# Kernel optimization log

Measured on AMD Instinct MI355X. Metric: run time of the kernel, lower is better.

The kernel has to match this reference:

```python
import jax, jax.numpy as jnp
import numpy as np

B, H, W, BLK = 32, 512, 512, 8
QF_MIN, QF_MAX, QF_BIAS = 2.0, 50.0, 0.0

_RGB2YCC = jnp.array([[0.299, 0.587, 0.114],
                      [-0.168736, -0.331264, 0.5],
                      [0.5, -0.418688, -0.081312]], jnp.float32)
_YCC_OFF = jnp.array([0.0, 128.0, 128.0], jnp.float32)

Y_QTB = jnp.array([16,11,10,16,24,40,51,61,12,12,14,19,26,58,60,55,14,13,16,24,40,57,69,56,
                   14,17,22,29,51,87,80,62,18,22,37,56,68,109,103,77,24,36,55,64,81,104,113,92,
                   49,64,78,87,103,121,120,101,72,92,95,98,112,100,103,99], jnp.float32).reshape(8, 8)
C_QTB = jnp.array([17,18,24,47,99,99,99,99,18,21,26,66,99,99,99,99,24,26,56,99,99,99,99,99,
                   47,66,99,99,99,99,99,99,99,99,99,99,99,99,99,99,99,99,99,99,99,99,99,99,
                   99,99,99,99,99,99,99,99,99,99,99,99,99,99,99,99], jnp.float32).reshape(8, 8)

# orthonormal 8x8 DCT-II matrix
_k = np.arange(8.0)[:, None]; _n = np.arange(8.0)[None, :]
_C = 0.5 * np.cos((2 * _n + 1) * _k * np.pi / 16.0)
_C[0] *= 1.0 / np.sqrt(2.0)
DCT_M = jnp.asarray(_C, jnp.float32)

# standard JPEG zig-zag raster order over the 64 coefficients of an 8x8 block
ZIGZAG = jnp.array([0,1,8,16,9,2,3,10,17,24,32,25,18,11,4,5,12,19,26,33,40,48,41,34,27,20,13,6,
                    7,14,21,28,35,42,49,56,57,50,43,36,29,22,15,23,30,37,44,51,58,59,52,45,38,31,
                    39,46,53,60,61,54,47,55,62,63], jnp.int32)


def hard_round(x):
    # straight-through round: forward = round(x), backward = identity
    return x + jax.lax.stop_gradient(jnp.round(x) - x)


def split_blocks(x):
    # [B,H,W] -> [B,H/8,W/8,8,8]
    b, h, w = x.shape
    return x.reshape(b, h // BLK, BLK, w // BLK, BLK).transpose(0, 1, 3, 2, 4)


def dct2d(x):
    # 2D DCT over the trailing 8x8 dims: C @ X @ C^T
    return jnp.einsum('ij,bnmjk,lk->bnmil', DCT_M, x, DCT_M)


def _norm01(e):
    mn = e.min(axis=(1, 2), keepdims=True)
    mx = e.max(axis=(1, 2), keepdims=True)
    return (e - mn) / (mx - mn + 1e-6)


def _ac_energy(d):
    # per-block log AC energy, shape [B,h8,w8]
    return jnp.log1p(jnp.sum(d * d, axis=(-2, -1)) - d[..., 0, 0] ** 2 + 1e-6)


def _forward(rgb):
    ycbcr = hard_round(jnp.einsum('bhwc,kc->bhwk', rgb, _RGB2YCC) + _YCC_OFF) - 128.0
    y_d = dct2d(split_blocks(ycbcr[..., 0]))
    cb_d = dct2d(split_blocks(ycbcr[..., 1]))
    cr_d = dct2d(split_blocks(ycbcr[..., 2]))

    # QFMapGenerator (default): per-block AC-energy rank in [0,1], upsampled to pixels
    rank = jnp.stack([_norm01(_ac_energy(y_d)),
                      _norm01(0.5 * (_ac_energy(cb_d) + _ac_energy(cr_d)))], axis=-1)  # [B,h8,w8,2]
    rank_px = jnp.repeat(jnp.repeat(rank, BLK, axis=1), BLK, axis=2)  # [B,H,W,2]

    # RankToQF
    enc_qf = jnp.clip(hard_round(QF_MIN + rank_px * (QF_MAX - QF_MIN) + QF_BIAS), QF_MIN, QF_MAX)
    y_qf_min = enc_qf[..., 0].min(axis=(1, 2), keepdims=True)
    y_qf_max = enc_qf[..., 0].max(axis=(1, 2), keepdims=True)
    c_qf_min = enc_qf[..., 1].min(axis=(1, 2), keepdims=True)
    c_qf_max = enc_qf[..., 1].max(axis=(1, 2), keepdims=True)

    # QFToScale: standard JPEG QF -> scale factor
    enc_scale = hard_round(jnp.where(enc_qf < 50.0, 5000.0 / enc_qf, 200.0 - 2.0 * enc_qf)) / 100.0

    sy = split_blocks(enc_scale[..., 0])  # [B,h8,w8,8,8]
    sc = split_blocks(enc_scale[..., 1])
    yq = hard_round(y_d / (sy * Y_QTB))
    cbq = hard_round(cb_d / (sc * C_QTB))
    crq = hard_round(cr_d / (sc * C_QTB))
    qdct = jnp.stack([yq, cbq, crq], axis=1)  # [B,3,h8,w8,8,8]

    nb = (H // BLK) * (W // BLK)
    flat = qdct.reshape(B, 3, nb, 64)
    # delta encode along the block axis
    delta = jnp.concatenate([flat[:, :, :1], flat[:, :, 1:] - flat[:, :, :-1]], axis=2)
    # zig-zag raster scan of the 64 coefficients
    zz = delta[..., ZIGZAG]
    blocks = jnp.log(jnp.abs(zz) + 1.0) / jnp.log(2.0)
    blocks = blocks.reshape(-1, 64)
    return qdct, blocks, enc_qf, enc_scale, y_qf_min, y_qf_max, c_qf_min, c_qf_max


def setup_inputs() -> dict:
    key = jax.random.key(0)
    rgb = jax.random.uniform(key, (B, H, W, 3), jnp.float32) * 255.0
    return {"rgb": rgb}


def reference(rgb):
    return _forward(rgb)
```

## Files before the change

### kernel.cpp

```cpp
#include <hip/hip_runtime.h>
#include <math.h>

#define BB 32
#define HH 512
#define WW 512
#define NB 4096
#define NTILES (BB * NB)
#define QD 25165824
#define PP 16777216
#define TAILOFF (2 * (size_t)QD + 2 * (size_t)PP)

__constant__ int c_zz[64] = {
    0,1,8,16,9,2,3,10,17,24,32,25,18,11,4,5,12,19,26,33,40,48,41,34,27,20,13,6,
    7,14,21,28,35,42,49,56,57,50,43,36,29,22,15,23,30,37,44,51,58,59,52,45,38,31,
    39,46,53,60,61,54,47,55,62,63};

struct CdArg { double v[64]; };
struct QArg  { float Cf[64]; double rqY[64]; double rqC[64]; };

__device__ __forceinline__ double qf_from_rank(double r) {
    double q = rint(2.0 + r * 48.0 + 0.0);
    return fmin(fmax(q, 2.0), 50.0);
}
__device__ __forceinline__ double scale_from_qf(double qf) {
    double s = (qf < 50.0) ? (5000.0 / qf) : (200.0 - 2.0 * qf);
    return rint(s) / 100.0;
}

__device__ __forceinline__ void stage_ycc(const float* __restrict__ rgb,
                                          int b, int i, int t,
                                          float (*planes)[8][512]) {
    const float* src = rgb + (size_t)(b * HH + i * 8) * WW * 3;
    int p0 = t * 16;
    alignas(16) float px[48];
    const float4* s4 = (const float4*)(src + (size_t)p0 * 3);
    #pragma unroll
    for (int k = 0; k < 12; ++k) ((float4*)px)[k] = s4[k];
    alignas(16) float yb[16], cb[16], cr[16];
    #pragma unroll
    for (int k = 0; k < 16; ++k) {
        double R = px[3 * k], G = px[3 * k + 1], Bv = px[3 * k + 2];
        yb[k] = (float)(rint(R * (double)0.299f     + G * (double)0.587f     + Bv * (double)0.114f)             - 128.0);
        cb[k] = (float)(rint(R * (double)-0.168736f + G * (double)-0.331264f + Bv * (double)0.5f       + 128.0) - 128.0);
        cr[k] = (float)(rint(R * (double)0.5f       + G * (double)-0.418688f + Bv * (double)-0.081312f + 128.0) - 128.0);
    }
    int r0 = p0 >> 9, c0 = p0 & 511;
    #pragma unroll
    for (int k = 0; k < 4; ++k) {
        *(float4*)&planes[0][r0][c0 + 4 * k] = ((float4*)yb)[k];
        *(float4*)&planes[1][r0][c0 + 4 * k] = ((float4*)cb)[k];
        *(float4*)&planes[2][r0][c0 + 4 * k] = ((float4*)cr)[k];
    }
}

__global__ __launch_bounds__(256, 2) void k_energy(const float* __restrict__ rgb,
                                                   CdArg A,
                                                   double* __restrict__ ey,
                                                   double* __restrict__ ec) {
    __shared__ __align__(16) float planes[3][8][512];
    __shared__ double ecomb[2][64];
    int b = blockIdx.x >> 6, i = blockIdx.x & 63;
    int t = threadIdx.x;
    stage_ycc(rgb, b, i, t, planes);
    __syncthreads();
    int ch = t >> 6, j = t & 63;
    if (ch < 3) {
        double U[8][8];
        #pragma unroll
        for (int r = 0; r < 8; ++r) {
            alignas(16) float xr[8];
            *(float4*)xr       = *(const float4*)&planes[ch][r][j * 8];
            *(float4*)(xr + 4) = *(const float4*)&planes[ch][r][j * 8 + 4];
            double xd[8];
            #pragma unroll
            for (int s = 0; s < 8; ++s) xd[s] = (double)xr[s];
            #pragma unroll
            for (int v = 0; v < 8; ++v) {
                double u = 0.0;
                #pragma unroll
                for (int s = 0; s < 8; ++s) u += xd[s] * A.v[v * 8 + s];
                U[r][v] = u;
            }
        }
        double sum = 0.0, dc = 0.0;
        #pragma unroll
        for (int u = 0; u < 8; ++u) {
            #pragma unroll
            for (int v = 0; v < 8; ++v) {
                double d = 0.0;
                #pragma unroll
                for (int r = 0; r < 8; ++r) d += A.v[u * 8 + r] * U[r][v];
                sum += d * d;
                if (u == 0 && v == 0) dc = d;
            }
        }
        double e = log1p(sum - dc * dc + 1e-6);
        if (ch == 0) ey[b * NB + i * 64 + j] = e;
        else ecomb[ch - 1][j] = e;
    }
    __syncthreads();
    if (t < 64) ec[b * NB + i * 64 + t] = 0.5 * (ecomb[0][t] + ecomb[1][t]);
}

__global__ __launch_bounds__(256) void k_minmax(const double* __restrict__ ey,
                                                const double* __restrict__ ec,
                                                double* __restrict__ mm,
                                                float* __restrict__ out_tail) {
    __shared__ double s0[256], s1[256], s2[256], s3[256];
    int b = blockIdx.x, tid = threadIdx.x;
    double mny = 1e300, mxy = -1e300, mnc = 1e300, mxc = -1e300;
    for (int n = tid; n < NB; n += 256) {
        double vy = ey[b * NB + n], vc = ec[b * NB + n];
        mny = fmin(mny, vy); mxy = fmax(mxy, vy);
        mnc = fmin(mnc, vc); mxc = fmax(mxc, vc);
    }
    s0[tid] = mny; s1[tid] = mxy; s2[tid] = mnc; s3[tid] = mxc;
    __syncthreads();
    for (int off = 128; off > 0; off >>= 1) {
        if (tid < off) {
            s0[tid] = fmin(s0[tid], s0[tid + off]);
            s1[tid] = fmax(s1[tid], s1[tid + off]);
            s2[tid] = fmin(s2[tid], s2[tid + off]);
            s3[tid] = fmax(s3[tid], s3[tid + off]);
        }
        __syncthreads();
    }
    if (tid == 0) {
        mm[b] = s0[0]; mm[32 + b] = s1[0]; mm[64 + b] = s2[0]; mm[96 + b] = s3[0];
        double ry = (s1[0] - s0[0]) / (s1[0] - s0[0] + 1e-6);
        double rc = (s3[0] - s2[0]) / (s3[0] - s2[0] + 1e-6);
        out_tail[b]      = (float)qf_from_rank(0.0);
        out_tail[32 + b] = (float)qf_from_rank(ry);
        out_tail[64 + b] = (float)qf_from_rank(0.0);
        out_tail[96 + b] = (float)qf_from_rank(rc);
    }
}

__global__ __launch_bounds__(256, 2) void k_quant(const float* __restrict__ rgb,
                                                  QArg A,
                                                  const double* __restrict__ ey,
                                                  const double* __restrict__ ec,
                                                  const double* __restrict__ mm,
                                                  float* __restrict__ out) {
    __shared__ __align__(16) float planes[3][8][512];
    int b = blockIdx.x >> 6, i = blockIdx.x & 63;
    int t = threadIdx.x;
    stage_ycc(rgb, b, i, t, planes);
    __syncthreads();
    int ch = t >> 6, j = t & 63;
    if (ch < 3) {
        int gt = b * NB + i * 64 + j;
        double eyv = ey[gt], ecv = ec[gt];
        double mny = mm[b], mxy = mm[32 + b], mnc = mm[64 + b], mxc = mm[96 + b];
        double ry = (eyv - mny) / (mxy - mny + 1e-6);
        double rc = (ecv - mnc) / (mxc - mnc + 1e-6);
        double qy = qf_from_rank(ry), qc = qf_from_rank(rc);
        double sy = scale_from_qf(qy), sc = scale_from_qf(qc);

        float U[8][8];
        #pragma unroll
        for (int r = 0; r < 8; ++r) {
            alignas(16) float xr[8];
            *(float4*)xr       = *(const float4*)&planes[ch][r][j * 8];
            *(float4*)(xr + 4) = *(const float4*)&planes[ch][r][j * 8 + 4];
            #pragma unroll
            for (int v = 0; v < 8; ++v) {
                float u = 0.0f;
                #pragma unroll
                for (int s = 0; s < 8; ++s) u += xr[s] * A.Cf[v * 8 + s];
                U[r][v] = u;
            }
        }
        double rinv = 1.0 / ((ch == 0) ? sy : sc);
        const double* rqt = (ch == 0) ? A.rqY : A.rqC;
        size_t qbase = (((size_t)b * 3 + ch) * NB + (size_t)(i * 64 + j)) * 64;
        #pragma unroll
        for (int u = 0; u < 8; ++u) {
            alignas(16) float orow[8];
            #pragma unroll
            for (int v = 0; v < 8; ++v) {
                float d = 0.0f;
                #pragma unroll
                for (int r = 0; r < 8; ++r) d += A.Cf[u * 8 + r] * U[r][v];
                orow[v] = (float)rint((double)d * (rqt[u * 8 + v] * rinv));
            }
            *(float4*)(out + qbase + u * 8)     = ((float4*)orow)[0];
            *(float4*)(out + qbase + u * 8 + 4) = ((float4*)orow)[1];
        }

        if (ch < 2) {
            float4 v4 = (ch == 0)
                ? make_float4((float)qy, (float)qc, (float)qy, (float)qc)
                : make_float4((float)sy, (float)sc, (float)sy, (float)sc);
            float* mbase = out + 2 * (size_t)QD + (ch ? PP : 0);
            size_t P = (size_t)(b * HH + i * 8) * WW + j * 8;
            #pragma unroll
            for (int rr = 0; rr < 8; ++rr) {
                float4* dst = (float4*)((float2*)mbase + P + (size_t)rr * WW);
                dst[0] = v4; dst[1] = v4; dst[2] = v4; dst[3] = v4;
            }
        }
    }
}

__global__ __launch_bounds__(256) void k_blocks(const float* __restrict__ q,
                                                float* __restrict__ ob) {
    int t = threadIdx.x;
    int row = blockIdx.x * 4 + (t >> 6);
    int lane = t & 63;
    int n = row & 4095;
    size_t base = (size_t)row * 64;
    float cur = q[base + lane];
    float prev = (n > 0) ? q[base - 64 + lane] : 0.0f;
    float dlt = cur - prev;
    float g = __shfl(dlt, c_zz[lane], 64);
    ob[base + lane] = log2f(fabsf(g) + 1.0f);
}

extern "C" void kernel_launch(void* const* d_in, const int* in_sizes, int n_in,
                              void* d_out, int out_size, void* d_ws, size_t ws_size,
                              hipStream_t stream) {
    const float* rgb = (const float*)d_in[0];
    float* out = (float*)d_out;
    double* ws = (double*)d_ws;
    double* ey = ws;
    double* ec = ws + (size_t)NTILES;
    double* mm = ws + 2 * (size_t)NTILES;

    static const double YQ[64] = {
        16,11,10,16,24,40,51,61, 12,12,14,19,26,58,60,55, 14,13,16,24,40,57,69,56,
        14,17,22,29,51,87,80,62, 18,22,37,56,68,109,103,77, 24,36,55,64,81,104,113,92,
        49,64,78,87,103,121,120,101, 72,92,95,98,112,100,103,99};
    static const double CQ[64] = {
        17,18,24,47,99,99,99,99, 18,21,26,66,99,99,99,99, 24,26,56,99,99,99,99,99,
        47,66,99,99,99,99,99,99, 99,99,99,99,99,99,99,99, 99,99,99,99,99,99,99,99,
        99,99,99,99,99,99,99,99, 99,99,99,99,99,99,99,99};

    CdArg ca; QArg qa;
    for (int k = 0; k < 8; ++k)
        for (int n = 0; n < 8; ++n) {
            double v = 0.5 * cos((2.0 * n + 1.0) * (double)k * M_PI / 16.0);
            if (k == 0) v *= 0.70710678118654752440;
            float f = (float)v;
            ca.v[k * 8 + n] = (double)f;
            qa.Cf[k * 8 + n] = f;
        }
    for (int k = 0; k < 64; ++k) { qa.rqY[k] = 1.0 / YQ[k]; qa.rqC[k] = 1.0 / CQ[k]; }

    dim3 blk(256);
    k_energy<<<BB * 64, blk, 0, stream>>>(rgb, ca, ey, ec);
    k_minmax<<<BB, blk, 0, stream>>>(ey, ec, mm, out + TAILOFF);
    k_quant<<<BB * 64, blk, 0, stream>>>(rgb, qa, ey, ec, mm, out);
    k_blocks<<<(BB * 3 * NB) / 4, blk, 0, stream>>>(out, out + QD);
}
```

Before: 523.3 us.

## Compute AC energy via Parseval, fuse delta/zigzag/log into quant kernel

The energy kernel no longer runs a double-precision DCT. Because the DCT is orthonormal, it gets AC energy from pixel-domain sums: sum of squares minus the squared sum over 64, using integer partial sums in shared memory. The quant kernel stages YCbCr as shorts and writes quantized coefficients to shared memory. It then computes the delta, zigzag and log2 blocks output in place, and a small fix-up kernel recomputes only the first block of each row, whose predecessor lies in another workgroup. Occupancy hints rise to 4, and the exact-arithmetic equivalence relies on integer rounded pixels and on float DCT matrix values being close to orthonormal.

After: 499.2 us. 4.6% less time.

```diff
diff --git a/kernel.cpp b/kernel.cpp
--- a/kernel.cpp
+++ b/kernel.cpp
@@ -5,18 +5,20 @@
 #define HH 512
 #define WW 512
 #define NB 4096
-#define NTILES (BB * NB)
 #define QD 25165824
 #define PP 16777216
 #define TAILOFF (2 * (size_t)QD + 2 * (size_t)PP)
 
+constexpr int ZZc[64] = {
+    0,1,8,16,9,2,3,10,17,24,32,25,18,11,4,5,12,19,26,33,40,48,41,34,27,20,13,6,
+    7,14,21,28,35,42,49,56,57,50,43,36,29,22,15,23,30,37,44,51,58,59,52,45,38,31,
+    39,46,53,60,61,54,47,55,62,63};
 __constant__ int c_zz[64] = {
     0,1,8,16,9,2,3,10,17,24,32,25,18,11,4,5,12,19,26,33,40,48,41,34,27,20,13,6,
     7,14,21,28,35,42,49,56,57,50,43,36,29,22,15,23,30,37,44,51,58,59,52,45,38,31,
     39,46,53,60,61,54,47,55,62,63};
 
-struct CdArg { double v[64]; };
-struct QArg  { float Cf[64]; double rqY[64]; double rqC[64]; };
+struct QArg { float Cf[64]; double rqY[64]; double rqC[64]; };
 
 __device__ __forceinline__ double qf_from_rank(double r) {
     double q = rint(2.0 + r * 48.0 + 0.0);
@@ -27,74 +29,55 @@
     return rint(s) / 100.0;
 }
 
-__device__ __forceinline__ void stage_ycc(const float* __restrict__ rgb,
-                                          int b, int i, int t,
-                                          float (*planes)[8][512]) {
-    const float* src = rgb + (size_t)(b * HH + i * 8) * WW * 3;
-    int p0 = t * 16;
-    alignas(16) float px[48];
+__device__ __forceinline__ void ycc16(const float* __restrict__ src, int p0,
+                                      int* y, int* cb, int* cr) {
+    float px[48];
     const float4* s4 = (const float4*)(src + (size_t)p0 * 3);
     #pragma unroll
     for (int k = 0; k < 12; ++k) ((float4*)px)[k] = s4[k];
-    alignas(16) float yb[16], cb[16], cr[16];
     #pragma unroll
     for (int k = 0; k < 16; ++k) {
         double R = px[3 * k], G = px[3 * k + 1], Bv = px[3 * k + 2];
-        yb[k] = (float)(rint(R * (double)0.299f     + G * (double)0.587f     + Bv * (double)0.114f)             - 128.0);
-        cb[k] = (float)(rint(R * (double)-0.168736f + G * (double)-0.331264f + Bv * (double)0.5f       + 128.0) - 128.0);
-        cr[k] = (float)(rint(R * (double)0.5f       + G * (double)-0.418688f + Bv * (double)-0.081312f + 128.0) - 128.0);
-    }
-    int r0 = p0 >> 9, c0 = p0 & 511;
-    #pragma unroll
-    for (int k = 0; k < 4; ++k) {
-        *(float4*)&planes[0][r0][c0 + 4 * k] = ((float4*)yb)[k];
-        *(float4*)&planes[1][r0][c0 + 4 * k] = ((float4*)cb)[k];
-        *(float4*)&planes[2][r0][c0 + 4 * k] = ((float4*)cr)[k];
-    }
-}
-
-__global__ __launch_bounds__(256, 2) void k_energy(const float* __restrict__ rgb,
-                                                   CdArg A,
+        y[k]  = (int)(rint(R * (double)0.299f     + G * (double)0.587f     + Bv * (double)0.114f)             - 128.0);
+        cb[k] = (int)(rint(R * (double)-0.168736f + G * (double)-0.331264f + Bv * (double)0.5f       + 128.0) - 128.0);
+        cr[k] = (int)(rint(R * (double)0.5f       + G * (double)-0.418688f + Bv * (double)-0.081312f + 128.0) - 128.0);
+    }
+}
+
+__global__ __launch_bounds__(256, 4) void k_energy(const float* __restrict__ rgb,
                                                    double* __restrict__ ey,
                                                    double* __restrict__ ec) {
-    __shared__ __align__(16) float planes[3][8][512];
+    __shared__ int4 part[3][8][32];
     __shared__ double ecomb[2][64];
-    int b = blockIdx.x >> 6, i = blockIdx.x & 63;
-    int t = threadIdx.x;
-    stage_ycc(rgb, b, i, t, planes);
+    int b = blockIdx.x >> 6, i = blockIdx.x & 63, t = threadIdx.x;
+    const float* src = rgb + (size_t)(b * HH + i * 8) * WW * 3;
+    {
+        int y[16], cb[16], cr[16];
+        ycc16(src, t * 16, y, cb, cr);
+        int s[3][2] = {{0,0},{0,0},{0,0}}, s2[3][2] = {{0,0},{0,0},{0,0}};
+        #pragma unroll
+        for (int k = 0; k < 16; ++k) {
+            int h = k >> 3;
+            s[0][h] += y[k];  s2[0][h] += y[k] * y[k];
+            s[1][h] += cb[k]; s2[1][h] += cb[k] * cb[k];
+            s[2][h] += cr[k]; s2[2][h] += cr[k] * cr[k];
+        }
+        int r0 = t >> 5, c = t & 31;
+        #pragma unroll
+        for (int ch = 0; ch < 3; ++ch)
+            part[ch][r0][c] = make_int4(s[ch][0], s2[ch][0], s[ch][1], s2[ch][1]);
+    }
     __syncthreads();
     int ch = t >> 6, j = t & 63;
     if (ch < 3) {
-        double U[8][8];
+        int S = 0, S2 = 0;
         #pragma unroll
         for (int r = 0; r < 8; ++r) {
-            alignas(16) float xr[8];
-            *(float4*)xr       = *(const float4*)&planes[ch][r][j * 8];
-            *(float4*)(xr + 4) = *(const float4*)&planes[ch][r][j * 8 + 4];
-            double xd[8];
-            #pragma unroll
-            for (int s = 0; s < 8; ++s) xd[s] = (double)xr[s];
-            #pragma unroll
-            for (int v = 0; v < 8; ++v) {
-                double u = 0.0;
-                #pragma unroll
-                for (int s = 0; s < 8; ++s) u += xd[s] * A.v[v * 8 + s];
-                U[r][v] = u;
-            }
-        }
-        double sum = 0.0, dc = 0.0;
-        #pragma unroll
-        for (int u = 0; u < 8; ++u) {
-            #pragma unroll
-            for (int v = 0; v < 8; ++v) {
-                double d = 0.0;
-                #pragma unroll
-                for (int r = 0; r < 8; ++r) d += A.v[u * 8 + r] * U[r][v];
-                sum += d * d;
-                if (u == 0 && v == 0) dc = d;
-            }
-        }
-        double e = log1p(sum - dc * dc + 1e-6);
+            const int2* p = (const int2*)&part[ch][r][j >> 1];
+            int2 v = p[j & 1];
+            S += v.x; S2 += v.y;
+        }
+        double e = log1p((double)S2 - (double)S * (double)S * (1.0 / 64.0) + 1e-6);
         if (ch == 0) ey[b * NB + i * 64 + j] = e;
         else ecomb[ch - 1][j] = e;
     }
@@ -136,33 +119,48 @@
     }
 }
 
-__global__ __launch_bounds__(256, 2) void k_quant(const float* __restrict__ rgb,
+__global__ __launch_bounds__(256, 4) void k_quant(const float* __restrict__ rgb,
                                                   QArg A,
                                                   const double* __restrict__ ey,
                                                   const double* __restrict__ ec,
                                                   const double* __restrict__ mm,
                                                   float* __restrict__ out) {
-    __shared__ __align__(16) float planes[3][8][512];
-    int b = blockIdx.x >> 6, i = blockIdx.x & 63;
-    int t = threadIdx.x;
-    stage_ycc(rgb, b, i, t, planes);
+    __shared__ __align__(16) short sm[13056];
+    int b = blockIdx.x >> 6, i = blockIdx.x & 63, t = threadIdx.x;
+    {
+        int y[16], cb[16], cr[16];
+        ycc16(rgb + (size_t)(b * HH + i * 8) * WW * 3, t * 16, y, cb, cr);
+        alignas(16) short yb[16], cbb[16], crb[16];
+        #pragma unroll
+        for (int k = 0; k < 16; ++k) {
+            yb[k] = (short)y[k]; cbb[k] = (short)cb[k]; crb[k] = (short)cr[k];
+        }
+        int4* d0 = (int4*)&sm[0 * 4096 + 16 * t];
+        int4* d1 = (int4*)&sm[1 * 4096 + 16 * t];
+        int4* d2 = (int4*)&sm[2 * 4096 + 16 * t];
+        d0[0] = ((int4*)yb)[0];  d0[1] = ((int4*)yb)[1];
+        d1[0] = ((int4*)cbb)[0]; d1[1] = ((int4*)cbb)[1];
+        d2[0] = ((int4*)crb)[0]; d2[1] = ((int4*)crb)[1];
+    }
     __syncthreads();
     int ch = t >> 6, j = t & 63;
+    float U[8][8];
+    double qy = 0, qc = 0, sy = 1, sc = 1;
     if (ch < 3) {
         int gt = b * NB + i * 64 + j;
         double eyv = ey[gt], ecv = ec[gt];
         double mny = mm[b], mxy = mm[32 + b], mnc = mm[64 + b], mxc = mm[96 + b];
         double ry = (eyv - mny) / (mxy - mny + 1e-6);
         double rc = (ecv - mnc) / (mxc - mnc + 1e-6);
-        double qy = qf_from_rank(ry), qc = qf_from_rank(rc);
-        double sy = scale_from_qf(qy), sc = scale_from_qf(qc);
-
-        float U[8][8];
+        qy = qf_from_rank(ry); qc = qf_from_rank(rc);
+        sy = scale_from_qf(qy); sc = scale_from_qf(qc);
         #pragma unroll
         for (int r = 0; r < 8; ++r) {
-            alignas(16) float xr[8];
-            *(float4*)xr       = *(const float4*)&planes[ch][r][j * 8];
-            *(float4*)(xr + 4) = *(const float4*)&planes[ch][r][j * 8 + 4];
+            alignas(16) short xs[8];
+            *(int4*)xs = *(const int4*)&sm[ch * 4096 + r * 512 + j * 8];
+            float xr[8];
+            #pragma unroll
+            for (int s = 0; s < 8; ++s) xr[s] = (float)xs[s];
             #pragma unroll
             for (int v = 0; v < 8; ++v) {
                 float u = 0.0f;
@@ -171,23 +169,49 @@
                 U[r][v] = u;
             }
         }
+    }
+    __syncthreads();
+    if (ch < 3) {
         double rinv = 1.0 / ((ch == 0) ? sy : sc);
         const double* rqt = (ch == 0) ? A.rqY : A.rqC;
         size_t qbase = (((size_t)b * 3 + ch) * NB + (size_t)(i * 64 + j)) * 64;
+        int sqb = (ch * 64 + j) * 66;
         #pragma unroll
         for (int u = 0; u < 8; ++u) {
             alignas(16) float orow[8];
+            alignas(4) short srow[8];
             #pragma unroll
             for (int v = 0; v < 8; ++v) {
                 float d = 0.0f;
                 #pragma unroll
                 for (int r = 0; r < 8; ++r) d += A.Cf[u * 8 + r] * U[r][v];
-                orow[v] = (float)rint((double)d * (rqt[u * 8 + v] * rinv));
+                float qv = (float)rint((double)d * (rqt[u * 8 + v] * rinv));
+                orow[v] = qv; srow[v] = (short)qv;
             }
             *(float4*)(out + qbase + u * 8)     = ((float4*)orow)[0];
             *(float4*)(out + qbase + u * 8 + 4) = ((float4*)orow)[1];
-        }
-
+            short2* sd = (short2*)&sm[sqb + u * 8];
+            sd[0] = ((short2*)srow)[0]; sd[1] = ((short2*)srow)[1];
+            sd[2] = ((short2*)srow)[2]; sd[3] = ((short2*)srow)[3];
+        }
+    }
+    __syncthreads();
+    if (ch < 3) {
+        int sqb = (ch * 64 + j) * 66;
+        size_t bbase = (size_t)QD + (((size_t)b * 3 + ch) * NB + (size_t)(i * 64 + j)) * 64;
+        #pragma unroll
+        for (int u = 0; u < 8; ++u) {
+            alignas(16) float bo[8];
+            #pragma unroll
+            for (int e = 0; e < 8; ++e) {
+                int zk = ZZc[u * 8 + e];
+                float cur = (float)sm[sqb + zk];
+                float prv = (j > 0) ? (float)sm[sqb - 66 + zk] : 0.0f;
+                bo[e] = log2f(fabsf(cur - prv) + 1.0f);
+            }
+            *(float4*)(out + bbase + u * 8)     = ((float4*)bo)[0];
+            *(float4*)(out + bbase + u * 8 + 4) = ((float4*)bo)[1];
+        }
         if (ch < 2) {
             float4 v4 = (ch == 0)
                 ? make_float4((float)qy, (float)qc, (float)qy, (float)qc)
@@ -203,18 +227,16 @@
     }
 }
 
-__global__ __launch_bounds__(256) void k_blocks(const float* __restrict__ q,
-                                                float* __restrict__ ob) {
-    int t = threadIdx.x;
-    int row = blockIdx.x * 4 + (t >> 6);
-    int lane = t & 63;
-    int n = row & 4095;
-    size_t base = (size_t)row * 64;
-    float cur = q[base + lane];
-    float prev = (n > 0) ? q[base - 64 + lane] : 0.0f;
-    float dlt = cur - prev;
-    float g = __shfl(dlt, c_zz[lane], 64);
-    ob[base + lane] = log2f(fabsf(g) + 1.0f);
+__global__ __launch_bounds__(256) void k_fix(const float* __restrict__ q,
+                                             float* __restrict__ ob) {
+    int idx = blockIdx.x * 256 + threadIdx.x;
+    int rid = idx >> 6, k = idx & 63;
+    int bch = rid >> 6;
+    int i = rid & 63;
+    size_t base = ((size_t)bch * NB + (size_t)i * 64) * 64;
+    float cur = q[base + c_zz[k]];
+    float prv = (i > 0) ? q[base - 64 + c_zz[k]] : 0.0f;
+    ob[base + k] = log2f(fabsf(cur - prv) + 1.0f);
 }
 
 extern "C" void kernel_launch(void* const* d_in, const int* in_sizes, int n_in,
@@ -224,8 +246,8 @@
     float* out = (float*)d_out;
     double* ws = (double*)d_ws;
     double* ey = ws;
-    double* ec = ws + (size_t)NTILES;
-    double* mm = ws + 2 * (size_t)NTILES;
+    double* ec = ws + (size_t)BB * NB;
+    double* mm = ws + 2 * (size_t)BB * NB;
 
     static const double YQ[64] = {
         16,11,10,16,24,40,51,61, 12,12,14,19,26,58,60,55, 14,13,16,24,40,57,69,56,
@@ -236,20 +258,18 @@
         47,66,99,99,99,99,99,99, 99,99,99,99,99,99,99,99, 99,99,99,99,99,99,99,99,
         99,99,99,99,99,99,99,99, 99,99,99,99,99,99,99,99};
 
-    CdArg ca; QArg qa;
+    QArg qa;
     for (int k = 0; k < 8; ++k)
         for (int n = 0; n < 8; ++n) {
             double v = 0.5 * cos((2.0 * n + 1.0) * (double)k * M_PI / 16.0);
             if (k == 0) v *= 0.70710678118654752440;
-            float f = (float)v;
-            ca.v[k * 8 + n] = (double)f;
-            qa.Cf[k * 8 + n] = f;
+            qa.Cf[k * 8 + n] = (float)v;
         }
     for (int k = 0; k < 64; ++k) { qa.rqY[k] = 1.0 / YQ[k]; qa.rqC[k] = 1.0 / CQ[k]; }
 
     dim3 blk(256);
-    k_energy<<<BB * 64, blk, 0, stream>>>(rgb, ca, ey, ec);
+    k_energy<<<BB * 64, blk, 0, stream>>>(rgb, ey, ec);
     k_minmax<<<BB, blk, 0, stream>>>(ey, ec, mm, out + TAILOFF);
     k_quant<<<BB * 64, blk, 0, stream>>>(rgb, qa, ey, ec, mm, out);
-    k_blocks<<<(BB * 3 * NB) / 4, blk, 0, stream>>>(out, out + QD);
-}
+    k_fix<<<(BB * 3 * 64 * 64) / 256, blk, 0, stream>>>(out, out + QD);
+}
```
